# Optimization experiments

Measured on AMD Instinct MI355X. Metric: run time of the kernel, lower is better.

Reference implementation:

```python
import jax, jax.numpy as jnp
import numpy as np

K_MASK = -2.3819763e38  # gemma masking constant


def apply_rope(inputs, positions, head_dim):
    # inputs: [B, T, N, H], positions: [B, T]
    half = head_dim // 2
    fraction = 2.0 * jnp.arange(half, dtype=jnp.float32) / head_dim
    timescale = 10000.0 ** fraction                      # [half]
    sinusoid = positions[..., None].astype(jnp.float32) / timescale  # [B, T, half]
    sin = jnp.sin(sinusoid)[:, :, None, :]               # [B, T, 1, half]
    cos = jnp.cos(sinusoid)[:, :, None, :]
    first, second = jnp.split(inputs, 2, axis=-1)
    out = jnp.concatenate([first * cos - second * sin,
                           second * cos + first * sin], axis=-1)
    return out.astype(inputs.dtype)


def setup_inputs() -> dict:
    key = jax.random.key(0)
    k0, k1, k2, k3 = jax.random.split(key, 4)
    B, T, D, N, H = 4, 1024, 2048, 16, 128
    x = jax.random.normal(k0, (B, T, D), dtype=jnp.float32)
    wq = jax.random.normal(k1, (N, D, H), dtype=jnp.float32) * 0.02
    wkv = jax.random.normal(k2, (2, 1, D, H), dtype=jnp.float32) * 0.02  # MQA: 1 kv head
    wo = jax.random.normal(k3, (N, H, D), dtype=jnp.float32) * 0.02
    segment_pos = jnp.broadcast_to(jnp.arange(T, dtype=jnp.int32), (B, T))
    attn_mask = jnp.broadcast_to(jnp.tril(jnp.ones((T, T), dtype=bool)), (B, T, T))
    return {"x": x, "wq": wq, "wkv": wkv, "wo": wo,
            "segment_pos": segment_pos, "attn_mask": attn_mask}


def reference(x, wq, wkv, wo, segment_pos, attn_mask):
    N, _, H = wq.shape
    # projections
    q = jnp.einsum('BTD,NDH->BTNH', x, wq)          # [B,T,N,H]
    kv = jnp.einsum('BSD,CKDH->CBSKH', x, wkv)      # [2,B,S,1,H]
    k, v = kv[0], kv[1]
    # RoPE + scaling
    q = apply_rope(q, segment_pos, H) * (H ** -0.5)
    k = apply_rope(k, segment_pos, H)
    # MQA head repeat: 1 kv head -> N heads
    k = jnp.repeat(k, N, axis=-2)                   # [B,S,N,H]
    v = jnp.repeat(v, N, axis=-2)
    # attention with manual masked softmax
    logits = jnp.einsum('BTNH,BSNH->BTNS', q, k)
    padded = jnp.where(attn_mask[:, :, None, :], logits, K_MASK)
    probs = jax.nn.softmax(padded, axis=-1).astype(k.dtype)
    encoded = jnp.einsum('BTNS,BSNH->BTNH', probs, v)
    return jnp.einsum('BTNH,NHD->BTD', encoded, wo)
```

## Files before the change

kernel.cpp:

```cpp
#include <hip/hip_runtime.h>
#include <cstdint>
#include <cstddef>

typedef unsigned short u16;
typedef __attribute__((ext_vector_type(8))) short bf16x8;
typedef __attribute__((ext_vector_type(4))) float f32x4;

#define B_ 4
#define T_ 1024
#define D_ 2048
#define N_ 16
#define H_ 128
#define BT_ (B_ * T_)
#define KMASK (-2.3819763e38f)

__device__ __forceinline__ u16 f2bf(float f) {
  uint32_t u = __builtin_bit_cast(uint32_t, f);
  u += 0x7FFFu + ((u >> 16) & 1u);
  return (u16)(u >> 16);
}
__device__ __forceinline__ float bf2f(uint32_t u) {
  return __builtin_bit_cast(float, u << 16);
}

__device__ __forceinline__ void gload16(const void* g, void* l) {
  __builtin_amdgcn_global_load_lds((const __attribute__((address_space(1))) void*)g,
                                   (__attribute__((address_space(3))) void*)l, 16, 0, 0);
}

__global__ __launch_bounds__(256) void convert_x_kernel(const float* __restrict__ x,
                                                        u16* __restrict__ xb) {
  int i = (blockIdx.x * 256 + threadIdx.x) * 8;
  float4 v0 = *(const float4*)(x + i);
  float4 v1 = *(const float4*)(x + i + 4);
  uint4 o;
  o.x = (uint32_t)f2bf(v0.x) | ((uint32_t)f2bf(v0.y) << 16);
  o.y = (uint32_t)f2bf(v0.z) | ((uint32_t)f2bf(v0.w) << 16);
  o.z = (uint32_t)f2bf(v1.x) | ((uint32_t)f2bf(v1.y) << 16);
  o.w = (uint32_t)f2bf(v1.z) | ((uint32_t)f2bf(v1.w) << 16);
  *(uint4*)(xb + i) = o;
}

__global__ __launch_bounds__(256) void transpose_kernel(const float* __restrict__ src,
                                                        u16* __restrict__ dst, int R, int C) {
  __shared__ float tile[32][33];
  const int z = blockIdx.z;
  const float* s = src + (size_t)z * R * C;
  u16* d = dst + (size_t)z * R * C;
  const int tx = threadIdx.x, ty = threadIdx.y;
  const int r0 = blockIdx.y * 32, c0 = blockIdx.x * 32;
#pragma unroll
  for (int i = 0; i < 4; ++i)
    tile[ty + i * 8][tx] = s[(size_t)(r0 + ty + i * 8) * C + (c0 + tx)];
  __syncthreads();
#pragma unroll
  for (int i = 0; i < 4; ++i)
    d[(size_t)(c0 + ty + i * 8) * R + (r0 + tx)] = f2bf(tile[tx][ty + i * 8]);
}

__global__ __launch_bounds__(256) void rope_table_kernel(float* __restrict__ costab,
                                                         float* __restrict__ sintab) {
  int idx = blockIdx.x * 256 + threadIdx.x;
  int p = idx >> 6, i = idx & 63;
  float ts = powf(10000.0f, (float)i * (1.0f / 64.0f));
  float ang = (float)p / ts;
  costab[idx] = cosf(ang);
  sintab[idx] = sinf(ang);
}

__global__ __launch_bounds__(256) void proj_gemm_kernel(
    const u16* __restrict__ xb, const u16* __restrict__ wqT, const u16* __restrict__ wkvT,
    u16* __restrict__ qraw, u16* __restrict__ kraw, u16* __restrict__ vT) {
  __shared__ alignas(16) u16 a_lds[128 * 64];
  __shared__ alignas(16) u16 b_lds[128 * 64];
  const int bid = blockIdx.x;
  const int newbid = (bid & 7) * 72 + (bid >> 3);
  const int y = newbid >> 5;
  const int m0 = (newbid & 31) * 128;
  const u16* Bt = (y < N_) ? (wqT + (size_t)y * H_ * D_) : (wkvT + (size_t)(y - N_) * H_ * D_);
  const int tid = threadIdx.x;
  const int w = tid >> 6, lane = tid & 63;
  const int g = lane >> 4, li = lane & 15;
  const int mrow = (w >> 1) * 64, wc = (w & 1) * 64;
  f32x4 acc[4][4];
#pragma unroll
  for (int i = 0; i < 4; ++i)
#pragma unroll
    for (int j = 0; j < 4; ++j) acc[i][j] = (f32x4){0.f, 0.f, 0.f, 0.f};

  for (int k0 = 0; k0 < D_; k0 += 64) {
    __syncthreads();
#pragma unroll
    for (int it = 0; it < 4; ++it) {
      int chunk = it * 256 + tid;
      int row = chunk >> 3, cu = chunk & 7;
      gload16(xb + (size_t)(m0 + row) * D_ + k0 + ((cu ^ (row & 7)) << 3), &a_lds[chunk * 8]);
    }
#pragma unroll
    for (int it = 0; it < 4; ++it) {
      int chunk = it * 256 + tid;
      int row = chunk >> 3, cu = chunk & 7;
      gload16(Bt + (size_t)row * D_ + k0 + ((cu ^ (row & 7)) << 3), &b_lds[chunk * 8]);
    }
    __syncthreads();
#pragma unroll
    for (int c2 = 0; c2 < 2; ++c2) {
      bf16x8 af[4], bfr[4];
#pragma unroll
      for (int i = 0; i < 4; ++i) {
        int row = mrow + i * 16 + li;
        af[i] = *(const bf16x8*)((const char*)a_lds +
                                 row * 128 + ((c2 * 64 + g * 16) ^ ((row & 7) << 4)));
      }
#pragma unroll
      for (int j = 0; j < 4; ++j) {
        int row = wc + j * 16 + li;
        bfr[j] = *(const bf16x8*)((const char*)b_lds +
                                  row * 128 + ((c2 * 64 + g * 16) ^ ((row & 7) << 4)));
      }
#pragma unroll
      for (int i = 0; i < 4; ++i)
#pragma unroll
        for (int j = 0; j < 4; ++j)
          acc[i][j] = __builtin_amdgcn_mfma_f32_16x16x32_bf16(af[i], bfr[j], acc[i][j], 0, 0, 0);
    }
  }

  const int b = m0 >> 10;
  if (y == N_ + 1) {
    const int tbase0 = (m0 & 1023) + mrow;
#pragma unroll
    for (int i = 0; i < 4; ++i) {
      int tbase = tbase0 + i * 16 + g * 4;
#pragma unroll
      for (int j = 0; j < 4; ++j) {
        int h = wc + j * 16 + li;
        ushort4 pk;
        pk.x = f2bf(acc[i][j][0]);
        pk.y = f2bf(acc[i][j][1]);
        pk.z = f2bf(acc[i][j][2]);
        pk.w = f2bf(acc[i][j][3]);
        *(ushort4*)(vT + ((size_t)(b * H_ + h)) * T_ + tbase) = pk;
      }
    }
  } else {
    size_t rowbase = (y < N_) ? ((size_t)(b * N_ + y) * T_ + (m0 & 1023)) : (size_t)m0;
    u16* dst0 = (y < N_) ? qraw : kraw;
#pragma unroll
    for (int i = 0; i < 4; ++i)
#pragma unroll
      for (int r = 0; r < 4; ++r) {
        int trow = mrow + i * 16 + g * 4 + r;
        u16* dst = dst0 + (rowbase + trow) * H_;
#pragma unroll
        for (int j = 0; j < 4; ++j) dst[wc + j * 16 + li] = f2bf(acc[i][j][r]);
      }
  }
}

__global__ __launch_bounds__(256) void rope_apply_k_kernel(
    const u16* __restrict__ kraw, const int* __restrict__ segment_pos,
    const float* __restrict__ costab, const float* __restrict__ sintab,
    u16* __restrict__ kb) {
  const int rid = blockIdx.x * 8 + (threadIdx.x >> 5);
  const int j = threadIdx.x & 31;
  const u16* src = kraw + (size_t)rid * H_;
  u16* dst = kb + (size_t)rid * H_;
  int p = segment_pos[rid];
  p = p < 0 ? 0 : (p > 1023 ? 1023 : p);
  uint32_t ua = *(const uint32_t*)(src + 2 * j);
  uint32_t ub = *(const uint32_t*)(src + 64 + 2 * j);
  float2 cv = *(const float2*)(costab + p * 64 + 2 * j);
  float2 sv = *(const float2*)(sintab + p * 64 + 2 * j);
  float f1a = bf2f(ua & 0xffffu), f1b = bf2f(ua >> 16);
  float f2a = bf2f(ub & 0xffffu), f2b = bf2f(ub >> 16);
  *(uint32_t*)(dst + 2 * j) =
      (uint32_t)f2bf(f1a * cv.x - f2a * sv.x) | ((uint32_t)f2bf(f1b * cv.y - f2b * sv.y) << 16);
  *(uint32_t*)(dst + 64 + 2 * j) =
      (uint32_t)f2bf(f2a * cv.x + f1a * sv.x) | ((uint32_t)f2bf(f2b * cv.y + f1b * sv.y) << 16);
}

__global__ __launch_bounds__(256) void attn_kernel(
    const u16* __restrict__ qraw, const u16* __restrict__ kb, const u16* __restrict__ vT,
    const int* __restrict__ segment_pos, const float* __restrict__ costab,
    const float* __restrict__ sintab, u16* __restrict__ enc) {
  __shared__ alignas(16) u16 k_lds[2][64 * 128];
  __shared__ alignas(16) u16 v_lds[128 * 64];
  __shared__ alignas(16) u16 p_lds[4 * 2 * 16 * 64];
  const int bx = blockIdx.x;
  const int j = bx >> 6;
  const int bn = bx & 63;
  const int b = bn >> 4, n = bn & 15;
  const int tid = threadIdx.x, w = tid >> 6, lane = tid & 63;
  const int g = lane >> 4, li = lane & 15;
  const int t0g[2] = {j * 64 + w * 16, (15 - j) * 64 + w * 16};

  bf16x8 qf[2][4];
  const float scale = 0.12751743342f;
#pragma unroll
  for (int u = 0; u < 2; ++u) {
    const int trow = t0g[u] + li;
    const u16* qrow = qraw + ((size_t)(b * N_ + n) * T_ + trow) * H_;
#pragma unroll
    for (int c = 0; c < 4; ++c) qf[u][c] = *(const bf16x8*)(qrow + c * 32 + g * 8);
    int p = segment_pos[b * T_ + trow];
    p = p < 0 ? 0 : (p > 1023 ? 1023 : p);
#pragma unroll
    for (int c = 0; c < 2; ++c) {
      const float* cp = costab + p * 64 + c * 32 + g * 8;
      const float* sp = sintab + p * 64 + c * 32 + g * 8;
      f32x4 cv0 = *(const f32x4*)cp, cv1 = *(const f32x4*)(cp + 4);
      f32x4 sv0 = *(const f32x4*)sp, sv1 = *(const f32x4*)(sp + 4);
#pragma unroll
      for (int e = 0; e < 8; ++e) {
        float cvv = e < 4 ? cv0[e] : cv1[e - 4];
        float svv = e < 4 ? sv0[e] : sv1[e - 4];
        float f1 = bf2f((u16)qf[u][c][e]);
        float f2 = bf2f((u16)qf[u][c + 2][e]);
        qf[u][c][e] = (short)f2bf((f1 * cvv - f2 * svv) * scale);
        qf[u][c + 2][e] = (short)f2bf((f2 * cvv + f1 * svv) * scale);
      }
    }
  }

  f32x4 o[2][8];
#pragma unroll
  for (int u = 0; u < 2; ++u)
#pragma unroll
    for (int hn = 0; hn < 8; ++hn) o[u][hn] = (f32x4){0.f, 0.f, 0.f, 0.f};
  float m[2] = {-3e38f, -3e38f}, lsum[2] = {0.f, 0.f};

  auto stageK = [&](int buf, int s0) {
#pragma unroll
    for (int it = 0; it < 4; ++it) {
      int chunk = it * 256 + tid;
      int row = chunk >> 4, cu = chunk & 15;
      gload16(kb + ((size_t)b * T_ + s0 + row) * H_ + ((cu ^ (row & 7)) << 3),
              &k_lds[buf][chunk * 8]);
    }
  };
  auto stageV = [&](int s0) {
#pragma unroll
    for (int it = 0; it < 4; ++it) {
      int chunk = it * 256 + tid;
      int row = chunk >> 3, cu = chunk & 7;
      gload16(vT + ((size_t)(b * H_ + row)) * T_ + s0 + ((cu ^ (row & 7)) << 3),
              &v_lds[chunk * 8]);
    }
  };

  const int nst = 16 - j;
  stageK(0, 0);
  int cur = 0;
  for (int st = 0; st < nst; ++st) {
    const int s0 = st * 64;
    const bool pre = (st + 1 < nst);
    stageV(s0);
    if (pre) stageK(cur ^ 1, s0 + 64);
    if (pre) asm volatile("s_waitcnt vmcnt(8)" ::: "memory");
    else     asm volatile("s_waitcnt vmcnt(4)" ::: "memory");
    __builtin_amdgcn_sched_barrier(0);
    __builtin_amdgcn_s_barrier();
    const bool actA = (st <= j);

    f32x4 sacc[2][4];
#pragma unroll
    for (int u = 0; u < 2; ++u)
#pragma unroll
      for (int fn = 0; fn < 4; ++fn) sacc[u][fn] = (f32x4){0.f, 0.f, 0.f, 0.f};
    __builtin_amdgcn_s_setprio(1);
#pragma unroll
    for (int c = 0; c < 4; ++c) {
      bf16x8 kf[4];
#pragma unroll
      for (int fn = 0; fn < 4; ++fn) {
        int row = fn * 16 + li;
        kf[fn] = *(const bf16x8*)((const char*)&k_lds[cur][0] +
                                  row * 256 + ((c * 64 + g * 16) ^ ((row & 7) << 4)));
      }
#pragma unroll
      for (int fn = 0; fn < 4; ++fn)
        sacc[1][fn] = __builtin_amdgcn_mfma_f32_16x16x32_bf16(kf[fn], qf[1][c], sacc[1][fn], 0, 0, 0);
      if (actA)
#pragma unroll
        for (int fn = 0; fn < 4; ++fn)
          sacc[0][fn] = __builtin_amdgcn_mfma_f32_16x16x32_bf16(kf[fn], qf[0][c], sacc[0][fn], 0, 0, 0);
    }
    __builtin_amdgcn_s_setprio(0);

#pragma unroll
    for (int u = 0; u < 2; ++u) {
      if (u == 0 && !actA) continue;
      const int t0 = t0g[u];
      const bool needmask = (u == 0) ? (st == j) : (st == nst - 1);
      if (needmask) {
        int trow = t0 + li;
#pragma unroll
        for (int fn = 0; fn < 4; ++fn)
#pragma unroll
          for (int r = 0; r < 4; ++r)
            if (s0 + fn * 16 + g * 4 + r > trow) sacc[u][fn][r] = KMASK;
      }
      float mx = -3e38f;
#pragma unroll
      for (int fn = 0; fn < 4; ++fn)
#pragma unroll
        for (int r = 0; r < 4; ++r) mx = fmaxf(mx, sacc[u][fn][r]);
      mx = fmaxf(mx, __shfl_xor(mx, 16, 64));
      mx = fmaxf(mx, __shfl_xor(mx, 32, 64));
      if (__any(mx - m[u] > 11.5f)) {
        float mn = fmaxf(m[u], mx);
        float alpha = exp2f(m[u] - mn);
        m[u] = mn;
        lsum[u] *= alpha;
#pragma unroll
        for (int r = 0; r < 4; ++r) {
          float ar = __shfl(alpha, g * 4 + r, 64);
#pragma unroll
          for (int hn = 0; hn < 8; ++hn) o[u][hn][r] *= ar;
        }
      }
      float ps = 0.f;
#pragma unroll
      for (int fn = 0; fn < 4; ++fn)
#pragma unroll
        for (int r = 0; r < 4; ++r) {
          float p = exp2f(sacc[u][fn][r] - m[u]);
          sacc[u][fn][r] = p;
          ps += p;
        }
      ps += __shfl_xor(ps, 16, 64);
      ps += __shfl_xor(ps, 32, 64);
      lsum[u] += ps;
      char* pbase = (char*)p_lds + (w * 2 + u) * 2048;
#pragma unroll
      for (int fn = 0; fn < 4; ++fn) {
        uint32_t w0, w1;
        asm("v_cvt_pk_bf16_f32 %0, %1, %2"
            : "=v"(w0) : "v"(sacc[u][fn][0]), "v"(sacc[u][fn][1]));
        asm("v_cvt_pk_bf16_f32 %0, %1, %2"
            : "=v"(w1) : "v"(sacc[u][fn][2]), "v"(sacc[u][fn][3]));
        uint2 pk2 = {w0, w1};
        *(uint2*)(pbase + li * 128 + ((fn * 32 + g * 8) ^ ((li & 7) << 4))) = pk2;
      }
    }

    if (pre) asm volatile("s_waitcnt vmcnt(4)" ::: "memory");
    else     asm volatile("s_waitcnt vmcnt(0)" ::: "memory");
    __builtin_amdgcn_sched_barrier(0);
    __builtin_amdgcn_s_barrier();

    __builtin_amdgcn_s_setprio(1);
#pragma unroll
    for (int c2 = 0; c2 < 2; ++c2) {
      bf16x8 pfB = *(const bf16x8*)((char*)p_lds + (w * 2 + 1) * 2048 + li * 128 +
                                    ((c2 * 64 + g * 16) ^ ((li & 7) << 4)));
      bf16x8 pfA;
      if (actA)
        pfA = *(const bf16x8*)((char*)p_lds + (w * 2 + 0) * 2048 + li * 128 +
                               ((c2 * 64 + g * 16) ^ ((li & 7) << 4)));
#pragma unroll
      for (int hn = 0; hn < 8; ++hn) {
        int hrow = hn * 16 + li;
        bf16x8 vf = *(const bf16x8*)((const char*)v_lds +
                                     hrow * 128 + ((c2 * 64 + g * 16) ^ ((li & 7) << 4)));
        o[1][hn] = __builtin_amdgcn_mfma_f32_16x16x32_bf16(pfB, vf, o[1][hn], 0, 0, 0);
        if (actA)
          o[0][hn] = __builtin_amdgcn_mfma_f32_16x16x32_bf16(pfA, vf, o[0][hn], 0, 0, 0);
      }
    }
    __builtin_amdgcn_s_setprio(0);
    __builtin_amdgcn_s_barrier();
    cur ^= 1;
  }

#pragma unroll
  for (int u = 0; u < 2; ++u)
#pragma unroll
    for (int r = 0; r < 4; ++r) {
      float lr = __shfl(lsum[u], g * 4 + r, 64);
      float inv = 1.0f / lr;
      int t = t0g[u] + g * 4 + r;
      u16* dst = enc + ((size_t)(b * T_ + t)) * (N_ * H_) + n * H_;
#pragma unroll
      for (int hn = 0; hn < 8; ++hn) dst[hn * 16 + li] = f2bf(o[u][hn][r] * inv);
    }
}

__global__ __launch_bounds__(256) void out_gemm_kernel(const u16* __restrict__ enc,
                                                       const u16* __restrict__ woT,
                                                       float* __restrict__ out) {
  __shared__ alignas(16) u16 a_lds[128 * 64];
  __shared__ alignas(16) u16 b_lds[128 * 64];
  const int bid = blockIdx.x;
  const int newbid = (bid & 7) * 64 + (bid >> 3);
  const int m0 = (newbid & 31) * 128;
  const int n0 = (newbid >> 5) * 128;
  const int tid = threadIdx.x, w = tid >> 6, lane = tid & 63;
  const int g = lane >> 4, li = lane & 15;
  const int mrow = (w >> 1) * 64, wc = (w & 1) * 64;
  f32x4 acc[4][4];
#pragma unroll
  for (int i = 0; i < 4; ++i)
#pragma unroll
    for (int j = 0; j < 4; ++j) acc[i][j] = (f32x4){0.f, 0.f, 0.f, 0.f};

  for (int k0 = 0; k0 < D_; k0 += 64) {
    __syncthreads();
#pragma unroll
    for (int it = 0; it < 4; ++it) {
      int chunk = it * 256 + tid;
      int row = chunk >> 3, cu = chunk & 7;
      gload16(enc + (size_t)(m0 + row) * D_ + k0 + ((cu ^ (row & 7)) << 3), &a_lds[chunk * 8]);
    }
#pragma unroll
    for (int it = 0; it < 4; ++it) {
      int chunk = it * 256 + tid;
      int row = chunk >> 3, cu = chunk & 7;
      gload16(woT + (size_t)(n0 + row) * D_ + k0 + ((cu ^ (row & 7)) << 3), &b_lds[chunk * 8]);
    }
    __syncthreads();
#pragma unroll
    for (int c2 = 0; c2 < 2; ++c2) {
      bf16x8 af[4], bfr[4];
#pragma unroll
      for (int i = 0; i < 4; ++i) {
        int row = mrow + i * 16 + li;
        af[i] = *(const bf16x8*)((const char*)a_lds +
                                 row * 128 + ((c2 * 64 + g * 16) ^ ((row & 7) << 4)));
      }
#pragma unroll
      for (int j = 0; j < 4; ++j) {
        int row = wc + j * 16 + li;
        bfr[j] = *(const bf16x8*)((const char*)b_lds +
                                  row * 128 + ((c2 * 64 + g * 16) ^ ((row & 7) << 4)));
      }
#pragma unroll
      for (int i = 0; i < 4; ++i)
#pragma unroll
        for (int j = 0; j < 4; ++j)
          acc[i][j] = __builtin_amdgcn_mfma_f32_16x16x32_bf16(af[i], bfr[j], acc[i][j], 0, 0, 0);
    }
  }
#pragma unroll
  for (int i = 0; i < 4; ++i)
#pragma unroll
    for (int r = 0; r < 4; ++r) {
      int bt = m0 + mrow + i * 16 + g * 4 + r;
      float* dst = out + (size_t)bt * D_ + n0 + wc;
#pragma unroll
      for (int j = 0; j < 4; ++j) dst[j * 16 + li] = acc[i][j][r];
    }
}

extern "C" void kernel_launch(void* const* d_in, const int* in_sizes, int n_in,
                              void* d_out, int out_size, void* d_ws, size_t ws_size,
                              hipStream_t stream) {
  const float* x = (const float*)d_in[0];
  const float* wq = (const float*)d_in[1];
  const float* wkv = (const float*)d_in[2];
  const float* wo = (const float*)d_in[3];
  const int* segment_pos = (const int*)d_in[4];
  float* out = (float*)d_out;

  char* ws = (char*)d_ws;
  size_t off = 0;
  auto alloc = [&](size_t bytes) -> void* {
    void* p = ws + off;
    off += (bytes + 255) & ~(size_t)255;
    return p;
  };
  u16* xb   = (u16*)alloc((size_t)BT_ * D_ * 2);
  u16* wqT  = (u16*)alloc((size_t)N_ * H_ * D_ * 2);
  u16* wkvT = (u16*)alloc((size_t)2 * H_ * D_ * 2);
  u16* woT  = (u16*)alloc((size_t)D_ * N_ * H_ * 2);
  u16* qraw = (u16*)alloc((size_t)B_ * N_ * T_ * H_ * 2);
  u16* kb   = (u16*)alloc((size_t)B_ * T_ * H_ * 2);
  u16* kraw = (u16*)alloc((size_t)B_ * T_ * H_ * 2);
  u16* vT   = (u16*)alloc((size_t)B_ * H_ * T_ * 2);
  u16* enc  = (u16*)alloc((size_t)BT_ * N_ * H_ * 2);
  float* costab = (float*)alloc(1024 * 64 * 4);
  float* sintab = (float*)alloc(1024 * 64 * 4);

  convert_x_kernel<<<BT_ * D_ / 8 / 256, 256, 0, stream>>>(x, xb);
  dim3 tb(32, 8);
  transpose_kernel<<<dim3(H_ / 32, D_ / 32, N_), tb, 0, stream>>>(wq, wqT, D_, H_);
  transpose_kernel<<<dim3(H_ / 32, D_ / 32, 2), tb, 0, stream>>>(wkv, wkvT, D_, H_);
  transpose_kernel<<<dim3(D_ / 32, D_ / 32, 1), tb, 0, stream>>>(wo, woT, N_ * H_, D_);
  rope_table_kernel<<<256, 256, 0, stream>>>(costab, sintab);
  proj_gemm_kernel<<<576, 256, 0, stream>>>(xb, wqT, wkvT, qraw, kraw, vT);
  rope_apply_k_kernel<<<BT_ / 8, 256, 0, stream>>>(kraw, segment_pos, costab, sintab, kb);
  attn_kernel<<<512, 256, 0, stream>>>(qraw, kb, vT, segment_pos, costab, sintab, enc);
  out_gemm_kernel<<<512, 256, 0, stream>>>(enc, woT, out);
}
```

Baseline: 198.1 us.

## Switch attention to 32x32x16 MFMA with S^T layout and register-resident P

Rewrites the attention inner loop to use 32x32x16 bf16 MFMAs with each wave owning 32 query rows as columns of a transposed score tile. Instead of handling two query stripes per wave, warps 0-1 take the early stripe and warps 2-3 the late stripe, so softmax statistics become per-lane and the row reductions need only one cross-half shuffle. The probability tile now stays in registers and is repacked with lane-xor shuffles instead of a round trip through LDS. The intent is fewer LDS accesses, fewer shuffles and denser MFMA issue. The trade-off is higher register pressure and load imbalance between the wave pairs, since the early-stripe waves go idle for most iterations.

```diff
diff --git a/kernel.cpp b/kernel.cpp
--- a/kernel.cpp
+++ b/kernel.cpp
@@ -5,6 +5,8 @@
 typedef unsigned short u16;
 typedef __attribute__((ext_vector_type(8))) short bf16x8;
 typedef __attribute__((ext_vector_type(4))) float f32x4;
+typedef __attribute__((ext_vector_type(16))) float f32x16;
+typedef __attribute__((ext_vector_type(4))) uint32_t u32x4;
 
 #define B_ 4
 #define T_ 1024
@@ -186,49 +188,46 @@
     const float* __restrict__ sintab, u16* __restrict__ enc) {
   __shared__ alignas(16) u16 k_lds[2][64 * 128];
   __shared__ alignas(16) u16 v_lds[128 * 64];
-  __shared__ alignas(16) u16 p_lds[4 * 2 * 16 * 64];
   const int bx = blockIdx.x;
   const int j = bx >> 6;
   const int bn = bx & 63;
   const int b = bn >> 4, n = bn & 15;
   const int tid = threadIdx.x, w = tid >> 6, lane = tid & 63;
-  const int g = lane >> 4, li = lane & 15;
-  const int t0g[2] = {j * 64 + w * 16, (15 - j) * 64 + w * 16};
-
-  bf16x8 qf[2][4];
-  const float scale = 0.12751743342f;
-#pragma unroll
-  for (int u = 0; u < 2; ++u) {
-    const int trow = t0g[u] + li;
-    const u16* qrow = qraw + ((size_t)(b * N_ + n) * T_ + trow) * H_;
-#pragma unroll
-    for (int c = 0; c < 4; ++c) qf[u][c] = *(const bf16x8*)(qrow + c * 32 + g * 8);
-    int p = segment_pos[b * T_ + trow];
+  const int l31 = lane & 31, hi = lane >> 5;
+  const int stripe = (w < 2) ? j : 15 - j;
+  const int t0w = stripe * 64 + (w & 1) * 32;
+  const int t = t0w + l31;
+  const int lastA = (w < 2) ? j : 15 - j;
+
+  bf16x8 qf[8];
+  {
+    const u16* qrow = qraw + ((size_t)(b * N_ + n) * T_ + t) * H_;
+#pragma unroll
+    for (int kc = 0; kc < 8; ++kc) qf[kc] = *(const bf16x8*)(qrow + kc * 16 + hi * 8);
+    int p = segment_pos[b * T_ + t];
     p = p < 0 ? 0 : (p > 1023 ? 1023 : p);
-#pragma unroll
-    for (int c = 0; c < 2; ++c) {
-      const float* cp = costab + p * 64 + c * 32 + g * 8;
-      const float* sp = sintab + p * 64 + c * 32 + g * 8;
-      f32x4 cv0 = *(const f32x4*)cp, cv1 = *(const f32x4*)(cp + 4);
-      f32x4 sv0 = *(const f32x4*)sp, sv1 = *(const f32x4*)(sp + 4);
+    const float scale = 0.12751743342f;
+#pragma unroll
+    for (int kc = 0; kc < 4; ++kc) {
+      const float* cp = costab + p * 64 + kc * 16 + hi * 8;
+      const float* sp = sintab + p * 64 + kc * 16 + hi * 8;
 #pragma unroll
       for (int e = 0; e < 8; ++e) {
-        float cvv = e < 4 ? cv0[e] : cv1[e - 4];
-        float svv = e < 4 ? sv0[e] : sv1[e - 4];
-        float f1 = bf2f((u16)qf[u][c][e]);
-        float f2 = bf2f((u16)qf[u][c + 2][e]);
-        qf[u][c][e] = (short)f2bf((f1 * cvv - f2 * svv) * scale);
-        qf[u][c + 2][e] = (short)f2bf((f2 * cvv + f1 * svv) * scale);
+        float cv = cp[e], sv = sp[e];
+        float f1 = bf2f((u16)qf[kc][e]);
+        float f2 = bf2f((u16)qf[kc + 4][e]);
+        qf[kc][e] = (short)f2bf((f1 * cv - f2 * sv) * scale);
+        qf[kc + 4][e] = (short)f2bf((f2 * cv + f1 * sv) * scale);
       }
     }
   }
 
-  f32x4 o[2][8];
-#pragma unroll
-  for (int u = 0; u < 2; ++u)
-#pragma unroll
-    for (int hn = 0; hn < 8; ++hn) o[u][hn] = (f32x4){0.f, 0.f, 0.f, 0.f};
-  float m[2] = {-3e38f, -3e38f}, lsum[2] = {0.f, 0.f};
+  f32x16 o[4];
+#pragma unroll
+  for (int hc = 0; hc < 4; ++hc)
+#pragma unroll
+    for (int r = 0; r < 16; ++r) o[hc][r] = 0.f;
+  float m_ = -3e38f, lsum = 0.f;
 
   auto stageK = [&](int buf, int s0) {
 #pragma unroll
@@ -261,88 +260,63 @@
     else     asm volatile("s_waitcnt vmcnt(4)" ::: "memory");
     __builtin_amdgcn_sched_barrier(0);
     __builtin_amdgcn_s_barrier();
-    const bool actA = (st <= j);
-
-    f32x4 sacc[2][4];
-#pragma unroll
-    for (int u = 0; u < 2; ++u)
-#pragma unroll
-      for (int fn = 0; fn < 4; ++fn) sacc[u][fn] = (f32x4){0.f, 0.f, 0.f, 0.f};
-    __builtin_amdgcn_s_setprio(1);
-#pragma unroll
-    for (int c = 0; c < 4; ++c) {
-      bf16x8 kf[4];
-#pragma unroll
-      for (int fn = 0; fn < 4; ++fn) {
-        int row = fn * 16 + li;
-        kf[fn] = *(const bf16x8*)((const char*)&k_lds[cur][0] +
-                                  row * 256 + ((c * 64 + g * 16) ^ ((row & 7) << 4)));
-      }
-#pragma unroll
-      for (int fn = 0; fn < 4; ++fn)
-        sacc[1][fn] = __builtin_amdgcn_mfma_f32_16x16x32_bf16(kf[fn], qf[1][c], sacc[1][fn], 0, 0, 0);
-      if (actA)
-#pragma unroll
-        for (int fn = 0; fn < 4; ++fn)
-          sacc[0][fn] = __builtin_amdgcn_mfma_f32_16x16x32_bf16(kf[fn], qf[0][c], sacc[0][fn], 0, 0, 0);
-    }
-    __builtin_amdgcn_s_setprio(0);
-
-#pragma unroll
-    for (int u = 0; u < 2; ++u) {
-      if (u == 0 && !actA) continue;
-      const int t0 = t0g[u];
-      const bool needmask = (u == 0) ? (st == j) : (st == nst - 1);
-      if (needmask) {
-        int trow = t0 + li;
-#pragma unroll
-        for (int fn = 0; fn < 4; ++fn)
-#pragma unroll
-          for (int r = 0; r < 4; ++r)
-            if (s0 + fn * 16 + g * 4 + r > trow) sacc[u][fn][r] = KMASK;
-      }
+
+    const bool act = (st <= lastA);
+    f32x16 sacc[2];
+    if (act) {
+#pragma unroll
+      for (int sub = 0; sub < 2; ++sub)
+#pragma unroll
+        for (int r = 0; r < 16; ++r) sacc[sub][r] = 0.f;
+      __builtin_amdgcn_s_setprio(1);
+#pragma unroll
+      for (int kc = 0; kc < 8; ++kc)
+#pragma unroll
+        for (int sub = 0; sub < 2; ++sub) {
+          int srow = sub * 32 + l31;
+          bf16x8 kf = *(const bf16x8*)((const char*)&k_lds[cur][0] + srow * 256 +
+                                       ((kc * 32 + hi * 16) ^ ((srow & 7) << 4)));
+          sacc[sub] = __builtin_amdgcn_mfma_f32_32x32x16_bf16(kf, qf[kc], sacc[sub], 0, 0, 0);
+        }
+      __builtin_amdgcn_s_setprio(0);
+
+      if (st == lastA) {
+#pragma unroll
+        for (int sub = 0; sub < 2; ++sub)
+#pragma unroll
+          for (int r = 0; r < 16; ++r) {
+            int s = s0 + sub * 32 + (r & 3) + 8 * (r >> 2) + 4 * hi;
+            if (s > t) sacc[sub][r] = KMASK;
+          }
+      }
+
       float mx = -3e38f;
 #pragma unroll
-      for (int fn = 0; fn < 4; ++fn)
-#pragma unroll
-        for (int r = 0; r < 4; ++r) mx = fmaxf(mx, sacc[u][fn][r]);
-      mx = fmaxf(mx, __shfl_xor(mx, 16, 64));
+      for (int sub = 0; sub < 2; ++sub)
+#pragma unroll
+        for (int r = 0; r < 16; ++r) mx = fmaxf(mx, sacc[sub][r]);
       mx = fmaxf(mx, __shfl_xor(mx, 32, 64));
-      if (__any(mx - m[u] > 11.5f)) {
-        float mn = fmaxf(m[u], mx);
-        float alpha = exp2f(m[u] - mn);
-        m[u] = mn;
-        lsum[u] *= alpha;
-#pragma unroll
-        for (int r = 0; r < 4; ++r) {
-          float ar = __shfl(alpha, g * 4 + r, 64);
-#pragma unroll
-          for (int hn = 0; hn < 8; ++hn) o[u][hn][r] *= ar;
+      if (__any(mx - m_ > 11.5f)) {
+        float mn = fmaxf(m_, mx);
+        float alpha = exp2f(m_ - mn);
+        m_ = mn;
+        lsum *= alpha;
+#pragma unroll
+        for (int hc = 0; hc < 4; ++hc)
+#pragma unroll
+          for (int r = 0; r < 16; ++r) o[hc][r] *= alpha;
+      }
+      float ps = 0.f;
+#pragma unroll
+      for (int sub = 0; sub < 2; ++sub)
+#pragma unroll
+        for (int r = 0; r < 16; ++r) {
+          float pv = exp2f(sacc[sub][r] - m_);
+          sacc[sub][r] = pv;
+          ps += pv;
         }
-      }
-      float ps = 0.f;
-#pragma unroll
-      for (int fn = 0; fn < 4; ++fn)
-#pragma unroll
-        for (int r = 0; r < 4; ++r) {
-          float p = exp2f(sacc[u][fn][r] - m[u]);
-          sacc[u][fn][r] = p;
-          ps += p;
-        }
-      ps += __shfl_xor(ps, 16, 64);
       ps += __shfl_xor(ps, 32, 64);
-      lsum[u] += ps;
-      char* pbase = (char*)p_lds + (w * 2 + u) * 2048;
-#pragma unroll
-      for (int fn = 0; fn < 4; ++fn) {
-        uint32_t w0, w1;
-        asm("v_cvt_pk_bf16_f32 %0, %1, %2"
-            : "=v"(w0) : "v"(sacc[u][fn][0]), "v"(sacc[u][fn][1]));
-        asm("v_cvt_pk_bf16_f32 %0, %1, %2"
-            : "=v"(w1) : "v"(sacc[u][fn][2]), "v"(sacc[u][fn][3]));
-        uint2 pk2 = {w0, w1};
-        *(uint2*)(pbase + li * 128 + ((fn * 32 + g * 8) ^ ((li & 7) << 4))) = pk2;
-      }
+      lsum += ps;
     }
 
     if (pre) asm volatile("s_waitcnt vmcnt(4)" ::: "memory");
@@ -350,40 +324,52 @@
     __builtin_amdgcn_sched_barrier(0);
     __builtin_amdgcn_s_barrier();
 
-    __builtin_amdgcn_s_setprio(1);
-#pragma unroll
-    for (int c2 = 0; c2 < 2; ++c2) {
-      bf16x8 pfB = *(const bf16x8*)((char*)p_lds + (w * 2 + 1) * 2048 + li * 128 +
-                                    ((c2 * 64 + g * 16) ^ ((li & 7) << 4)));
-      bf16x8 pfA;
-      if (actA)
-        pfA = *(const bf16x8*)((char*)p_lds + (w * 2 + 0) * 2048 + li * 128 +
-                               ((c2 * 64 + g * 16) ^ ((li & 7) << 4)));
-#pragma unroll
-      for (int hn = 0; hn < 8; ++hn) {
-        int hrow = hn * 16 + li;
-        bf16x8 vf = *(const bf16x8*)((const char*)v_lds +
-                                     hrow * 128 + ((c2 * 64 + g * 16) ^ ((li & 7) << 4)));
-        o[1][hn] = __builtin_amdgcn_mfma_f32_16x16x32_bf16(pfB, vf, o[1][hn], 0, 0, 0);
-        if (actA)
-          o[0][hn] = __builtin_amdgcn_mfma_f32_16x16x32_bf16(pfA, vf, o[0][hn], 0, 0, 0);
-      }
-    }
-    __builtin_amdgcn_s_setprio(0);
+    if (act) {
+      __builtin_amdgcn_s_setprio(1);
+#pragma unroll
+      for (int sc = 0; sc < 4; ++sc) {
+        const int sub = sc >> 1, rb = (sc & 1) * 8;
+        uint32_t a0, a1, b0, b1;
+        asm("v_cvt_pk_bf16_f32 %0, %1, %2" : "=v"(a0) : "v"(sacc[sub][rb + 0]), "v"(sacc[sub][rb + 1]));
+        asm("v_cvt_pk_bf16_f32 %0, %1, %2" : "=v"(a1) : "v"(sacc[sub][rb + 2]), "v"(sacc[sub][rb + 3]));
+        asm("v_cvt_pk_bf16_f32 %0, %1, %2" : "=v"(b0) : "v"(sacc[sub][rb + 4]), "v"(sacc[sub][rb + 5]));
+        asm("v_cvt_pk_bf16_f32 %0, %1, %2" : "=v"(b1) : "v"(sacc[sub][rb + 6]), "v"(sacc[sub][rb + 7]));
+        uint32_t pa0 = (uint32_t)__shfl_xor((int)a0, 32, 64);
+        uint32_t pa1 = (uint32_t)__shfl_xor((int)a1, 32, 64);
+        uint32_t pb0 = (uint32_t)__shfl_xor((int)b0, 32, 64);
+        uint32_t pb1 = (uint32_t)__shfl_xor((int)b1, 32, 64);
+        uint32_t d0 = hi ? pb0 : a0;
+        uint32_t d1 = hi ? pb1 : a1;
+        uint32_t d2 = hi ? b0 : pa0;
+        uint32_t d3 = hi ? b1 : pa1;
+        u32x4 pdv = (u32x4){d0, d1, d2, d3};
+        bf16x8 pf = __builtin_bit_cast(bf16x8, pdv);
+#pragma unroll
+        for (int hc = 0; hc < 4; ++hc) {
+          int hrow = hc * 32 + l31;
+          bf16x8 vf = *(const bf16x8*)((const char*)v_lds + hrow * 128 +
+                                       ((sc * 32 + hi * 16) ^ ((hrow & 7) << 4)));
+          o[hc] = __builtin_amdgcn_mfma_f32_32x32x16_bf16(vf, pf, o[hc], 0, 0, 0);
+        }
+      }
+      __builtin_amdgcn_s_setprio(0);
+    }
     __builtin_amdgcn_s_barrier();
     cur ^= 1;
   }
 
-#pragma unroll
-  for (int u = 0; u < 2; ++u)
-#pragma unroll
-    for (int r = 0; r < 4; ++r) {
-      float lr = __shfl(lsum[u], g * 4 + r, 64);
-      float inv = 1.0f / lr;
-      int t = t0g[u] + g * 4 + r;
-      u16* dst = enc + ((size_t)(b * T_ + t)) * (N_ * H_) + n * H_;
-#pragma unroll
-      for (int hn = 0; hn < 8; ++hn) dst[hn * 16 + li] = f2bf(o[u][hn][r] * inv);
+  float inv = 1.0f / lsum;
+  u16* dst = enc + ((size_t)(b * T_ + t)) * (N_ * H_) + n * H_;
+#pragma unroll
+  for (int hc = 0; hc < 4; ++hc)
+#pragma unroll
+    for (int rq = 0; rq < 4; ++rq) {
+      ushort4 pk;
+      pk.x = f2bf(o[hc][rq * 4 + 0] * inv);
+      pk.y = f2bf(o[hc][rq * 4 + 1] * inv);
+      pk.z = f2bf(o[hc][rq * 4 + 2] * inv);
+      pk.w = f2bf(o[hc][rq * 4 + 3] * inv);
+      *(ushort4*)(dst + hc * 32 + rq * 8 + hi * 4) = pk;
     }
 }
 
```

Result: slower. 202.6 us (median of 2 runs) (+2.3%).
